# Kernel optimization log

Hardware: AMD Instinct MI355X
Metric: run time of the kernel (lower is better)

## Reference

```python
import jax, jax.numpy as jnp
import numpy as np
import math

H = 128      # hidden_size
B = 4        # bsz
N = 32       # bsz * num_doc_per_q
L = 128      # doc_len


def setup_inputs() -> dict:
    key = jax.random.key(0)
    ks = jax.random.split(key, 7)
    word_ent_info = jax.random.normal(ks[0], (N, L, H), dtype=jnp.float32)
    word_ent_info_mask = jax.random.randint(ks[1], (N, L), 0, 2, dtype=jnp.int32)
    doc = jax.random.normal(ks[2], (N, L, H), dtype=jnp.float32)
    doc_mask = jax.random.randint(ks[3], (N, L), 0, 2, dtype=jnp.int32)
    q_for_text = jax.random.normal(ks[4], (B, H), dtype=jnp.float32)
    # nn.Linear(3H, H): weight [H, 3H], bias [H]
    W1 = jax.random.normal(ks[5], (H, 3 * H), dtype=jnp.float32) / math.sqrt(3 * H)
    b1 = jnp.zeros((H,), dtype=jnp.float32)
    # nn.Linear(H, 1): weight [1, H], bias [1]
    w2 = jax.random.normal(ks[6], (1, H), dtype=jnp.float32) / math.sqrt(H)
    b2 = jnp.zeros((1,), dtype=jnp.float32)
    return {"word_ent_info": word_ent_info, "word_ent_info_mask": word_ent_info_mask,
            "doc": doc, "doc_mask": doc_mask, "q_for_text": q_for_text,
            "W1": W1, "b1": b1, "w2": w2, "b2": b2}


def reference(word_ent_info, word_ent_info_mask, doc, doc_mask, q_for_text, W1, b1, w2, b2):
    n, l, h = doc.shape
    bsz = q_for_text.shape[0]
    dt = doc.dtype

    # word_ent_infoagg = mask^T @ word_ent_info -> [N, H]
    m = word_ent_info_mask.astype(dt)
    ent_agg = jnp.einsum('nl,nlh->nh', m, word_ent_info)

    # q expanded to one row per document: [N, H]
    q_exp = jnp.repeat(q_for_text, n // bsz, axis=0)

    # Split W1 over the concat([doc_self, ent_agg, q_agg]) feature axis.
    # score_pre[n,j,k,:] = W1a @ (doc_j*doc_k) + W1b @ (doc_j*ent_agg) + W1c @ (doc_k*q)
    W1a, W1b, W1c = jnp.split(W1, 3, axis=1)        # each [H, H]
    A = jnp.einsum('nje,nke,ge->njkg', doc, doc, W1a)          # [N,L,L,H]
    Bt = jnp.einsum('nje,ge->njg', doc * ent_agg[:, None, :], W1b)  # [N,L,H]
    Ct = jnp.einsum('nke,ge->nkg', doc * q_exp[:, None, :], W1c)    # [N,L,H]
    hid = jnp.tanh(A + Bt[:, :, None, :] + Ct[:, None, :, :] + b1)  # [N,L,L,H]

    score = (jnp.einsum('njkg,g->njk', hid, w2[0]) + b2[0]) / math.sqrt(h)

    dm = doc_mask.astype(dt)
    score_mask = dm[:, :, None] * dm[:, None, :]     # [N,L,L]
    score = jnp.where(score_mask == 0.0, jnp.asarray(-1e9, dt), score)
    w = jax.nn.softmax(score, axis=-1) * score_mask
    doc_ent_enc = jnp.einsum('njk,nkh->njh', w, doc)  # [N,L,H]
    return doc_ent_enc
```

## Files before the change

### kernel.cpp

```cpp
#include <hip/hip_runtime.h>
#include <hip/hip_bf16.h>
#include <math.h>

#define Hh 128
#define Nn 32
#define Ll 128
#define W1S 384
#define PAD 136

typedef __attribute__((ext_vector_type(8))) short short8;
typedef __attribute__((ext_vector_type(4))) float floatx4;

__device__ __forceinline__ unsigned short f2bf(float x) {
  __hip_bfloat16 h = __float2bfloat16(x);
  return __builtin_bit_cast(unsigned short, h);
}
__device__ __forceinline__ float bf2f(short s) {
  unsigned int u = ((unsigned int)(unsigned short)s) << 16;
  return __builtin_bit_cast(float, u);
}
__device__ __forceinline__ short8 pack8(float4 a, float4 b) {
  short8 r;
  r[0] = (short)f2bf(a.x); r[1] = (short)f2bf(a.y);
  r[2] = (short)f2bf(a.z); r[3] = (short)f2bf(a.w);
  r[4] = (short)f2bf(b.x); r[5] = (short)f2bf(b.y);
  r[6] = (short)f2bf(b.z); r[7] = (short)f2bf(b.w);
  return r;
}

__launch_bounds__(256, 2)
__global__ void k_prep(const float* __restrict__ wei, const int* __restrict__ wmask,
                       const float* __restrict__ doc, const float* __restrict__ q,
                       const float* __restrict__ W1, const float* __restrict__ b1,
                       float* __restrict__ Bt, float* __restrict__ Ct) {
  __shared__ __align__(16) short Wsb[Hh * PAD];
  __shared__ __align__(16) short docb[64 * PAD];
  __shared__ __align__(16) float red[2][Hh];
  __shared__ __align__(16) float scale[Hh];

  int b = blockIdx.x;
  int n = b >> 2, which = (b >> 1) & 1, mh = b & 1;
  int tid = threadIdx.x;
  const float* docn = doc + (size_t)n * Ll * Hh;
  int e8 = (tid & 15) * 8;

  float4 dreg[4][2];
#pragma unroll
  for (int p = 0; p < 4; ++p) {
    int row = mh * 64 + p * 16 + (tid >> 4);
    const float4* dp = (const float4*)(docn + (size_t)row * Hh + e8);
    dreg[p][0] = dp[0]; dreg[p][1] = dp[1];
  }
#pragma unroll
  for (int p = 0; p < 8; ++p) {
    int row = p * 16 + (tid >> 4);
    const float4* wp = (const float4*)(W1 + (size_t)row * W1S + (which + 1) * Hh + e8);
    *(short8*)(Wsb + row * PAD + e8) = pack8(wp[0], wp[1]);
  }
  if (which == 1) {
    if (tid < Hh) scale[tid] = q[(n >> 3) * Hh + tid];
  } else {
    int e = tid & 127, halfl = tid >> 7;
    const float* wp = wei + (size_t)n * Ll * Hh + (size_t)halfl * 64 * Hh + e;
    const int* mp = wmask + n * Ll + halfl * 64;
    float a = 0.f;
#pragma unroll 16
    for (int l = 0; l < 64; ++l) a = fmaf((float)mp[l], wp[(size_t)l * Hh], a);
    red[halfl][e] = a;
  }
  __syncthreads();
  if (which == 0 && tid < Hh) scale[tid] = red[0][tid] + red[1][tid];
  __syncthreads();

  {
    float s[8];
#pragma unroll
    for (int i = 0; i < 8; ++i) s[i] = scale[e8 + i];
#pragma unroll
    for (int p = 0; p < 4; ++p) {
      int r = p * 16 + (tid >> 4);
      float4 a = dreg[p][0], bq = dreg[p][1];
      a.x *= s[0]; a.y *= s[1]; a.z *= s[2]; a.w *= s[3];
      bq.x *= s[4]; bq.y *= s[5]; bq.z *= s[6]; bq.w *= s[7];
      *(short8*)(docb + r * PAD + e8) = pack8(a, bq);
    }
  }
  __syncthreads();

  int lane = tid & 63, w = tid >> 6;
  int l15 = lane & 15, quad = lane >> 4;
  floatx4 acc[8];
#pragma unroll
  for (int nt = 0; nt < 8; ++nt) acc[nt] = (floatx4){0.f, 0.f, 0.f, 0.f};
#pragma unroll
  for (int c = 0; c < 4; ++c) {
    int eo = c * 32 + quad * 8;
    short8 af = *(const short8*)(docb + (w * 16 + l15) * PAD + eo);
    short8 bfr[8];
#pragma unroll
    for (int nt = 0; nt < 8; ++nt)
      bfr[nt] = *(const short8*)(Wsb + (nt * 16 + l15) * PAD + eo);
#pragma unroll
    for (int nt = 0; nt < 8; ++nt)
      acc[nt] = __builtin_amdgcn_mfma_f32_16x16x32_bf16(af, bfr[nt], acc[nt], 0, 0, 0);
  }

  float* outp = (which ? Ct : Bt) + (size_t)n * Ll * Hh;
#pragma unroll
  for (int nt = 0; nt < 8; ++nt) {
    int g = nt * 16 + l15;
    float badd = which ? 0.f : b1[g];
#pragma unroll
    for (int r = 0; r < 4; ++r) {
      int k = mh * 64 + w * 16 + quad * 4 + r;
      outp[(size_t)k * Hh + g] = acc[nt][r] + badd;
    }
  }
}

__launch_bounds__(512, 6)
__global__ void k_main(const float* __restrict__ doc, const int* __restrict__ dmask,
                       const float* __restrict__ W1,
                       const float* __restrict__ w2, const float* __restrict__ b2,
                       const float* __restrict__ Bt, const float* __restrict__ Ct,
                       float* __restrict__ out) {
  __shared__ __align__(16) short As[Hh * PAD];
  __shared__ __align__(16) float sc[Ll];
  __shared__ __align__(16) float scw[Ll];

  int bid = blockIdx.x;
  int n = bid & 31, j = bid >> 5;
  int tid = threadIdx.x;
  const float* docn = doc + (size_t)n * Ll * Hh;
  size_t orow = ((size_t)n * Ll + j) * Hh;

  if (dmask[n * Ll + j] == 0) {
    if (tid < Hh) out[orow + tid] = 0.f;
    return;
  }

  int e8 = (tid & 15) * 8;
#pragma unroll
  for (int p = 0; p < 4; ++p) {
    int row = p * 32 + (tid >> 4);
    const float4* wp = (const float4*)(W1 + (size_t)row * W1S + e8);
    *(short8*)(As + row * PAD + e8) = pack8(wp[0], wp[1]);
  }

  int lane = tid & 63, w = tid >> 6;
  int l15 = lane & 15, quad = lane >> 4;

  short8 af[4];
  {
    const float* drow = docn + (size_t)(w * 16 + l15) * Hh;
    const float* jrow = docn + (size_t)j * Hh;
#pragma unroll
    for (int c = 0; c < 4; ++c) {
      int eo = c * 32 + quad * 8;
      const float4* dp = (const float4*)(drow + eo);
      const float4* jp = (const float4*)(jrow + eo);
      float4 d0 = dp[0], d1 = dp[1];
      float4 j0 = jp[0], j1 = jp[1];
      d0.x *= j0.x; d0.y *= j0.y; d0.z *= j0.z; d0.w *= j0.w;
      d1.x *= j1.x; d1.y *= j1.y; d1.z *= j1.z; d1.w *= j1.w;
      af[c] = pack8(d0, d1);
    }
  }
  __syncthreads();

  floatx4 acc[8];
#pragma unroll
  for (int nt = 0; nt < 8; ++nt) acc[nt] = (floatx4){0.f, 0.f, 0.f, 0.f};
#pragma unroll
  for (int c = 0; c < 4; ++c) {
    int eo = c * 32 + quad * 8;
#pragma unroll
    for (int nt = 0; nt < 8; ++nt) {
      short8 bfr = *(const short8*)(As + (nt * 16 + l15) * PAD + eo);
      acc[nt] = __builtin_amdgcn_mfma_f32_16x16x32_bf16(af[c], bfr, acc[nt], 0, 0, 0);
    }
  }

  const float c2 = 2.885390081777927f;
  float bbc[8], w2r[8];
  const float* btrow = Bt + orow;
#pragma unroll
  for (int nt = 0; nt < 8; ++nt) {
    int g = nt * 16 + l15;
    bbc[nt] = btrow[g] * c2;
    w2r[nt] = w2[g];
  }
  const float* ctn = Ct + (size_t)n * Ll * Hh;
#pragma unroll
  for (int r = 0; r < 4; ++r) {
    int k = w * 16 + quad * 4 + r;
    const float* ctp = ctn + (size_t)k * Hh + l15;
    float p = 0.f;
#pragma unroll
    for (int nt = 0; nt < 8; ++nt) {
      float s = acc[nt][r] + ctp[nt * 16];
      float a2 = fmaf(s, c2, bbc[nt]);
      float e = exp2f(a2);
      float th = fmaf(-2.f, __builtin_amdgcn_rcpf(e + 1.f), 1.f);
      p = fmaf(th, w2r[nt], p);
    }
    p += __shfl_xor(p, 1);
    p += __shfl_xor(p, 2);
    p += __shfl_xor(p, 4);
    p += __shfl_xor(p, 8);
    if (l15 == 0) sc[k] = p;
  }
  __syncthreads();

  {
    float b2v = b2[0];
    const float inv = 0.088388347648318447f;
    const int* dmn = dmask + n * Ll;
    int m0 = dmn[lane], m1 = dmn[lane + 64];
    float s0 = (sc[lane] + b2v) * inv;
    float s1 = (sc[lane + 64] + b2v) * inv;
    s0 = m0 ? s0 : -1e9f;
    s1 = m1 ? s1 : -1e9f;
    float mx = fmaxf(s0, s1);
#pragma unroll
    for (int off = 32; off; off >>= 1) mx = fmaxf(mx, __shfl_xor(mx, off));
    float ex0 = __expf(s0 - mx), ex1 = __expf(s1 - mx);
    float sm = ex0 + ex1;
#pragma unroll
    for (int off = 32; off; off >>= 1) sm += __shfl_xor(sm, off);
    float rden = 1.f / sm;
    scw[lane] = m0 ? ex0 * rden : 0.f;
    scw[lane + 64] = m1 ? ex1 * rden : 0.f;
  }
  __syncthreads();

  float* ored = (float*)As;
  int halfk = tid >> 7, h = tid & 127;
  const float* dbase = docn + (size_t)halfk * 32 * Hh + h;
  float o = 0.f;
#pragma unroll 8
  for (int kk = 0; kk < 32; ++kk)
    o = fmaf(scw[halfk * 32 + kk], dbase[(size_t)kk * Hh], o);
  ored[halfk * Hh + h] = o;
  __syncthreads();
  if (tid < Ll)
    out[orow + tid] = ored[tid] + ored[Hh + tid] + ored[2 * Hh + tid] + ored[3 * Hh + tid];
}

extern "C" void kernel_launch(void* const* d_in, const int* in_sizes, int n_in,
                              void* d_out, int out_size, void* d_ws, size_t ws_size,
                              hipStream_t stream) {
  const float* wei   = (const float*)d_in[0];
  const int*   wmask = (const int*)d_in[1];
  const float* doc   = (const float*)d_in[2];
  const int*   dmask = (const int*)d_in[3];
  const float* q     = (const float*)d_in[4];
  const float* W1    = (const float*)d_in[5];
  const float* b1    = (const float*)d_in[6];
  const float* w2    = (const float*)d_in[7];
  const float* b2    = (const float*)d_in[8];
  float* out = (float*)d_out;

  float* ws = (float*)d_ws;
  float* Bt = ws;
  float* Ct = Bt + (size_t)Nn * Ll * Hh;

  k_prep<<<Nn * 4, 256, 0, stream>>>(wei, wmask, doc, q, W1, b1, Bt, Ct);
  k_main<<<Nn * Ll, 512, 0, stream>>>(doc, dmask, W1, w2, b2, Bt, Ct, out);
}
```

Before: 132.2 us.

## Compact unmasked query rows and process four per block in k_main

Each block now builds a compacted list of unmasked j rows using ballot and popcount, zero-fills masked rows, and handles up to four valid j rows. The W1a slice and the bf16 doc tile are staged into shared memory once per block, and the final weighted sum over doc is batched across four rows. This is meant to cut wasted blocks on masked rows, amortise W1/doc loading across rows, and shrink the grid from 4096 to 1024 blocks. The cost is more shared memory, lower occupancy (launch bounds 4), and extra bf16 rounding of doc before the elementwise product.

```diff
diff --git a/kernel.cpp b/kernel.cpp
--- a/kernel.cpp
+++ b/kernel.cpp
@@ -71,7 +71,6 @@
   __syncthreads();
   if (which == 0 && tid < Hh) scale[tid] = red[0][tid] + red[1][tid];
   __syncthreads();
-
   {
     float s[8];
 #pragma unroll
@@ -118,26 +117,45 @@
   }
 }
 
-__launch_bounds__(512, 6)
+__launch_bounds__(512, 4)
 __global__ void k_main(const float* __restrict__ doc, const int* __restrict__ dmask,
                        const float* __restrict__ W1,
                        const float* __restrict__ w2, const float* __restrict__ b2,
                        const float* __restrict__ Bt, const float* __restrict__ Ct,
                        float* __restrict__ out) {
   __shared__ __align__(16) short As[Hh * PAD];
-  __shared__ __align__(16) float sc[Ll];
-  __shared__ __align__(16) float scw[Ll];
+  __shared__ __align__(16) short docb[Hh * PAD];
+  __shared__ __align__(16) float sc[4][Ll];
+  __shared__ __align__(16) float scw[4][Ll];
+  __shared__ int jl[Ll], ml[Ll], cnts[4];
 
   int bid = blockIdx.x;
-  int n = bid & 31, j = bid >> 5;
+  int n = bid & 31, t = bid >> 5;
   int tid = threadIdx.x;
+  int lane = tid & 63, wv = tid >> 6;
   const float* docn = doc + (size_t)n * Ll * Hh;
-  size_t orow = ((size_t)n * Ll + j) * Hh;
-
-  if (dmask[n * Ll + j] == 0) {
-    if (tid < Hh) out[orow + tid] = 0.f;
-    return;
-  }
+  const int* dmn = dmask + n * Ll;
+
+  int jme = -1, mflag = 0, pre = 0;
+  if (wv < 2) {
+    jme = (wv << 6) + lane;
+    mflag = dmn[jme] != 0;
+    unsigned long long bal = __ballot(mflag);
+    pre = __popcll(bal & ((1ull << lane) - 1ull));
+    if (lane == 0) { int tot = __popcll(bal); cnts[wv] = tot; cnts[2 + wv] = 64 - tot; }
+  }
+  __syncthreads();
+  int cnt = cnts[0] + cnts[1];
+  if (wv == 0) { if (mflag) jl[pre] = jme; else ml[lane - pre] = jme; }
+  else if (wv == 1) { if (mflag) jl[cnts[0] + pre] = jme; else ml[cnts[2] + (lane - pre)] = jme; }
+  __syncthreads();
+
+  {
+    int rr = tid >> 7, h = tid & 127;
+    int mi = 4 * t + rr;
+    if (mi < Ll - cnt) out[((size_t)n * Ll + ml[mi]) * Hh + h] = 0.f;
+  }
+  if (4 * t >= cnt) return;
 
   int e8 = (tid & 15) * 8;
 #pragma unroll
@@ -145,106 +163,140 @@
     int row = p * 32 + (tid >> 4);
     const float4* wp = (const float4*)(W1 + (size_t)row * W1S + e8);
     *(short8*)(As + row * PAD + e8) = pack8(wp[0], wp[1]);
-  }
-
-  int lane = tid & 63, w = tid >> 6;
+    const float4* dp = (const float4*)(docn + (size_t)row * Hh + e8);
+    *(short8*)(docb + row * PAD + e8) = pack8(dp[0], dp[1]);
+  }
+  __syncthreads();
+
   int l15 = lane & 15, quad = lane >> 4;
 
-  short8 af[4];
-  {
-    const float* drow = docn + (size_t)(w * 16 + l15) * Hh;
+  short8 draw[4];
+#pragma unroll
+  for (int c = 0; c < 4; ++c)
+    draw[c] = *(const short8*)(docb + (wv * 16 + l15) * PAD + c * 32 + quad * 8);
+
+  float w2r[8];
+#pragma unroll
+  for (int nt = 0; nt < 8; ++nt) w2r[nt] = w2[nt * 16 + l15];
+
+  const float c2 = 2.885390081777927f;
+  const float* ctn = Ct + (size_t)n * Ll * Hh;
+
+  for (int jj = 0; jj < 4; ++jj) {
+    int idx = 4 * t + jj;
+    if (idx >= cnt) break;
+    int j = jl[idx];
     const float* jrow = docn + (size_t)j * Hh;
+
+    floatx4 acc[8];
+#pragma unroll
+    for (int nt = 0; nt < 8; ++nt) acc[nt] = (floatx4){0.f, 0.f, 0.f, 0.f};
 #pragma unroll
     for (int c = 0; c < 4; ++c) {
       int eo = c * 32 + quad * 8;
-      const float4* dp = (const float4*)(drow + eo);
       const float4* jp = (const float4*)(jrow + eo);
-      float4 d0 = dp[0], d1 = dp[1];
       float4 j0 = jp[0], j1 = jp[1];
-      d0.x *= j0.x; d0.y *= j0.y; d0.z *= j0.z; d0.w *= j0.w;
-      d1.x *= j1.x; d1.y *= j1.y; d1.z *= j1.z; d1.w *= j1.w;
-      af[c] = pack8(d0, d1);
-    }
-  }
-  __syncthreads();
-
-  floatx4 acc[8];
-#pragma unroll
-  for (int nt = 0; nt < 8; ++nt) acc[nt] = (floatx4){0.f, 0.f, 0.f, 0.f};
-#pragma unroll
-  for (int c = 0; c < 4; ++c) {
-    int eo = c * 32 + quad * 8;
-#pragma unroll
-    for (int nt = 0; nt < 8; ++nt) {
-      short8 bfr = *(const short8*)(As + (nt * 16 + l15) * PAD + eo);
-      acc[nt] = __builtin_amdgcn_mfma_f32_16x16x32_bf16(af[c], bfr, acc[nt], 0, 0, 0);
-    }
-  }
-
-  const float c2 = 2.885390081777927f;
-  float bbc[8], w2r[8];
-  const float* btrow = Bt + orow;
-#pragma unroll
-  for (int nt = 0; nt < 8; ++nt) {
-    int g = nt * 16 + l15;
-    bbc[nt] = btrow[g] * c2;
-    w2r[nt] = w2[g];
-  }
-  const float* ctn = Ct + (size_t)n * Ll * Hh;
-#pragma unroll
-  for (int r = 0; r < 4; ++r) {
-    int k = w * 16 + quad * 4 + r;
-    const float* ctp = ctn + (size_t)k * Hh + l15;
-    float p = 0.f;
-#pragma unroll
-    for (int nt = 0; nt < 8; ++nt) {
-      float s = acc[nt][r] + ctp[nt * 16];
-      float a2 = fmaf(s, c2, bbc[nt]);
-      float e = exp2f(a2);
-      float th = fmaf(-2.f, __builtin_amdgcn_rcpf(e + 1.f), 1.f);
-      p = fmaf(th, w2r[nt], p);
-    }
-    p += __shfl_xor(p, 1);
-    p += __shfl_xor(p, 2);
-    p += __shfl_xor(p, 4);
-    p += __shfl_xor(p, 8);
-    if (l15 == 0) sc[k] = p;
-  }
-  __syncthreads();
-
+      float4 ta, tb;
+      ta.x = bf2f(draw[c][0]) * j0.x; ta.y = bf2f(draw[c][1]) * j0.y;
+      ta.z = bf2f(draw[c][2]) * j0.z; ta.w = bf2f(draw[c][3]) * j0.w;
+      tb.x = bf2f(draw[c][4]) * j1.x; tb.y = bf2f(draw[c][5]) * j1.y;
+      tb.z = bf2f(draw[c][6]) * j1.z; tb.w = bf2f(draw[c][7]) * j1.w;
+      short8 af = pack8(ta, tb);
+#pragma unroll
+      for (int nt = 0; nt < 8; ++nt) {
+        short8 bfr = *(const short8*)(As + (nt * 16 + l15) * PAD + eo);
+        acc[nt] = __builtin_amdgcn_mfma_f32_16x16x32_bf16(af, bfr, acc[nt], 0, 0, 0);
+      }
+    }
+
+    float bbc[8];
+    const float* btrow = Bt + ((size_t)n * Ll + j) * Hh;
+#pragma unroll
+    for (int nt = 0; nt < 8; ++nt) bbc[nt] = btrow[nt * 16 + l15] * c2;
+#pragma unroll
+    for (int r = 0; r < 4; ++r) {
+      int k = wv * 16 + quad * 4 + r;
+      const float* ctp = ctn + (size_t)k * Hh + l15;
+      float p = 0.f;
+#pragma unroll
+      for (int nt = 0; nt < 8; ++nt) {
+        float s = acc[nt][r] + ctp[nt * 16];
+        float a2 = fmaf(s, c2, bbc[nt]);
+        float e = exp2f(a2);
+        float th = fmaf(-2.f, __builtin_amdgcn_rcpf(e + 1.f), 1.f);
+        p = fmaf(th, w2r[nt], p);
+      }
+      p += __shfl_xor(p, 1);
+      p += __shfl_xor(p, 2);
+      p += __shfl_xor(p, 4);
+      p += __shfl_xor(p, 8);
+      if (l15 == 0) sc[jj][k] = p;
+    }
+  }
+  __syncthreads();
+
+  if (wv < 4) {
+    int idx = 4 * t + wv;
+    if (idx < cnt) {
+      float b2v = b2[0];
+      const float inv = 0.088388347648318447f;
+      int m0 = dmn[lane], m1 = dmn[lane + 64];
+      float s0 = (sc[wv][lane] + b2v) * inv;
+      float s1 = (sc[wv][lane + 64] + b2v) * inv;
+      s0 = m0 ? s0 : -1e9f;
+      s1 = m1 ? s1 : -1e9f;
+      float mx = fmaxf(s0, s1);
+#pragma unroll
+      for (int off = 32; off; off >>= 1) mx = fmaxf(mx, __shfl_xor(mx, off));
+      float ex0 = __expf(s0 - mx), ex1 = __expf(s1 - mx);
+      float sm = ex0 + ex1;
+#pragma unroll
+      for (int off = 32; off; off >>= 1) sm += __shfl_xor(sm, off);
+      float rden = 1.f / sm;
+      scw[wv][lane] = m0 ? ex0 * rden : 0.f;
+      scw[wv][lane + 64] = m1 ? ex1 * rden : 0.f;
+    } else {
+      scw[wv][lane] = 0.f;
+      scw[wv][lane + 64] = 0.f;
+    }
+  }
+  __syncthreads();
+
+  float* ored = (float*)As;
   {
-    float b2v = b2[0];
-    const float inv = 0.088388347648318447f;
-    const int* dmn = dmask + n * Ll;
-    int m0 = dmn[lane], m1 = dmn[lane + 64];
-    float s0 = (sc[lane] + b2v) * inv;
-    float s1 = (sc[lane + 64] + b2v) * inv;
-    s0 = m0 ? s0 : -1e9f;
-    s1 = m1 ? s1 : -1e9f;
-    float mx = fmaxf(s0, s1);
-#pragma unroll
-    for (int off = 32; off; off >>= 1) mx = fmaxf(mx, __shfl_xor(mx, off));
-    float ex0 = __expf(s0 - mx), ex1 = __expf(s1 - mx);
-    float sm = ex0 + ex1;
-#pragma unroll
-    for (int off = 32; off; off >>= 1) sm += __shfl_xor(sm, off);
-    float rden = 1.f / sm;
-    scw[lane] = m0 ? ex0 * rden : 0.f;
-    scw[lane + 64] = m1 ? ex1 * rden : 0.f;
-  }
-  __syncthreads();
-
-  float* ored = (float*)As;
-  int halfk = tid >> 7, h = tid & 127;
-  const float* dbase = docn + (size_t)halfk * 32 * Hh + h;
-  float o = 0.f;
-#pragma unroll 8
-  for (int kk = 0; kk < 32; ++kk)
-    o = fmaf(scw[halfk * 32 + kk], dbase[(size_t)kk * Hh], o);
-  ored[halfk * Hh + h] = o;
-  __syncthreads();
-  if (tid < Ll)
-    out[orow + tid] = ored[tid] + ored[Hh + tid] + ored[2 * Hh + tid] + ored[3 * Hh + tid];
+    int halfk = tid >> 7, h = tid & 127;
+    const float* dbase = docn + (size_t)halfk * 32 * Hh + h;
+    float o0 = 0.f, o1 = 0.f, o2 = 0.f, o3 = 0.f;
+#pragma unroll
+    for (int k4 = 0; k4 < 8; ++k4) {
+      float4 s0 = *(const float4*)&scw[0][halfk * 32 + k4 * 4];
+      float4 s1 = *(const float4*)&scw[1][halfk * 32 + k4 * 4];
+      float4 s2 = *(const float4*)&scw[2][halfk * 32 + k4 * 4];
+      float4 s3 = *(const float4*)&scw[3][halfk * 32 + k4 * 4];
+      float d0 = dbase[(size_t)(k4 * 4 + 0) * Hh];
+      float d1 = dbase[(size_t)(k4 * 4 + 1) * Hh];
+      float d2 = dbase[(size_t)(k4 * 4 + 2) * Hh];
+      float d3 = dbase[(size_t)(k4 * 4 + 3) * Hh];
+      o0 = fmaf(s0.x, d0, o0); o0 = fmaf(s0.y, d1, o0); o0 = fmaf(s0.z, d2, o0); o0 = fmaf(s0.w, d3, o0);
+      o1 = fmaf(s1.x, d0, o1); o1 = fmaf(s1.y, d1, o1); o1 = fmaf(s1.z, d2, o1); o1 = fmaf(s1.w, d3, o1);
+      o2 = fmaf(s2.x, d0, o2); o2 = fmaf(s2.y, d1, o2); o2 = fmaf(s2.z, d2, o2); o2 = fmaf(s2.w, d3, o2);
+      o3 = fmaf(s3.x, d0, o3); o3 = fmaf(s3.y, d1, o3); o3 = fmaf(s3.z, d2, o3); o3 = fmaf(s3.w, d3, o3);
+    }
+    ored[(halfk * 4 + 0) * Hh + h] = o0;
+    ored[(halfk * 4 + 1) * Hh + h] = o1;
+    ored[(halfk * 4 + 2) * Hh + h] = o2;
+    ored[(halfk * 4 + 3) * Hh + h] = o3;
+  }
+  __syncthreads();
+  {
+    int jj2 = tid >> 7, h = tid & 127;
+    int idx = 4 * t + jj2;
+    if (idx < cnt) {
+      float v = ored[(0 * 4 + jj2) * Hh + h] + ored[(1 * 4 + jj2) * Hh + h] +
+                ored[(2 * 4 + jj2) * Hh + h] + ored[(3 * 4 + jj2) * Hh + h];
+      out[((size_t)n * Ll + jl[idx]) * Hh + h] = v;
+    }
+  }
 }
 
 extern "C" void kernel_launch(void* const* d_in, const int* in_sizes, int n_in,
@@ -266,5 +318,5 @@
   float* Ct = Bt + (size_t)Nn * Ll * Hh;
 
   k_prep<<<Nn * 4, 256, 0, stream>>>(wei, wmask, doc, q, W1, b1, Bt, Ct);
-  k_main<<<Nn * Ll, 512, 0, stream>>>(doc, dmask, W1, w2, b2, Bt, Ct, out);
-}
+  k_main<<<Nn * 32, 512, 0, stream>>>(doc, dmask, W1, w2, b2, Bt, Ct, out);
+}
```

Result: no change. 130.5 us (-1.3%).

## Stage doc and W1a in LDS as fp16 halves, compute products with packed fp16

Applied to the files above, without the earlier changes.

k_main now loads W1a and the document block into shared memory as fp16 in two 64-column chunks. Each wave forms the doc_j*doc_k products with packed fp16 vector multiplies read from LDS and feeds them to fp16 MFMA, replacing bf16 MFMA on products computed in fp32 registers. This makes the global loads coalesced row-chunk reads instead of per-lane strided rows, and uses fp16 for more mantissa precision. In exchange it adds an extra barrier and LDS traffic, and the products are formed in fp16, which risks overflow or precision loss.

```diff
diff --git a/kernel.cpp b/kernel.cpp
--- a/kernel.cpp
+++ b/kernel.cpp
@@ -7,17 +7,16 @@
 #define Ll 128
 #define W1S 384
 #define PAD 136
+#define EP 64
+#define SP 72
 
 typedef __attribute__((ext_vector_type(8))) short short8;
 typedef __attribute__((ext_vector_type(4))) float floatx4;
+typedef __attribute__((ext_vector_type(8))) _Float16 f16x8;
 
 __device__ __forceinline__ unsigned short f2bf(float x) {
   __hip_bfloat16 h = __float2bfloat16(x);
   return __builtin_bit_cast(unsigned short, h);
-}
-__device__ __forceinline__ float bf2f(short s) {
-  unsigned int u = ((unsigned int)(unsigned short)s) << 16;
-  return __builtin_bit_cast(float, u);
 }
 __device__ __forceinline__ short8 pack8(float4 a, float4 b) {
   short8 r;
@@ -25,6 +24,14 @@
   r[2] = (short)f2bf(a.z); r[3] = (short)f2bf(a.w);
   r[4] = (short)f2bf(b.x); r[5] = (short)f2bf(b.y);
   r[6] = (short)f2bf(b.z); r[7] = (short)f2bf(b.w);
+  return r;
+}
+__device__ __forceinline__ f16x8 cvt8h(float4 a, float4 b) {
+  f16x8 r;
+  r[0] = (_Float16)a.x; r[1] = (_Float16)a.y;
+  r[2] = (_Float16)a.z; r[3] = (_Float16)a.w;
+  r[4] = (_Float16)b.x; r[5] = (_Float16)b.y;
+  r[6] = (_Float16)b.z; r[7] = (_Float16)b.w;
   return r;
 }
 
@@ -71,7 +78,6 @@
   __syncthreads();
   if (which == 0 && tid < Hh) scale[tid] = red[0][tid] + red[1][tid];
   __syncthreads();
-
   {
     float s[8];
 #pragma unroll
@@ -124,7 +130,8 @@
                        const float* __restrict__ w2, const float* __restrict__ b2,
                        const float* __restrict__ Bt, const float* __restrict__ Ct,
                        float* __restrict__ out) {
-  __shared__ __align__(16) short As[Hh * PAD];
+  __shared__ __align__(16) _Float16 As[Hh * SP];
+  __shared__ __align__(16) _Float16 Bs[Hh * SP];
   __shared__ __align__(16) float sc[Ll];
   __shared__ __align__(16) float scw[Ll];
 
@@ -139,45 +146,39 @@
     return;
   }
 
-  int e8 = (tid & 15) * 8;
-#pragma unroll
-  for (int p = 0; p < 4; ++p) {
-    int row = p * 32 + (tid >> 4);
-    const float4* wp = (const float4*)(W1 + (size_t)row * W1S + e8);
-    *(short8*)(As + row * PAD + e8) = pack8(wp[0], wp[1]);
-  }
-
-  int lane = tid & 63, w = tid >> 6;
+  int lane = tid & 63, wv = tid >> 6;
   int l15 = lane & 15, quad = lane >> 4;
-
-  short8 af[4];
-  {
-    const float* drow = docn + (size_t)(w * 16 + l15) * Hh;
-    const float* jrow = docn + (size_t)j * Hh;
-#pragma unroll
-    for (int c = 0; c < 4; ++c) {
+  int grow = tid >> 2, seg = (tid & 3) * 16;
+
+  floatx4 acc[8];
+#pragma unroll
+  for (int nt = 0; nt < 8; ++nt) acc[nt] = (floatx4){0.f, 0.f, 0.f, 0.f};
+
+#pragma unroll
+  for (int p = 0; p < 2; ++p) {
+    if (p) __syncthreads();
+    {
+      const float4* dsrc = (const float4*)(docn + (size_t)grow * Hh + p * EP + seg);
+      const float4* wsrc = (const float4*)(W1 + (size_t)grow * W1S + p * EP + seg);
+      float4 d0 = dsrc[0], d1 = dsrc[1], d2 = dsrc[2], d3 = dsrc[3];
+      float4 w0 = wsrc[0], w1 = wsrc[1], w2v = wsrc[2], w3 = wsrc[3];
+      *(f16x8*)(Bs + grow * SP + seg) = cvt8h(d0, d1);
+      *(f16x8*)(Bs + grow * SP + seg + 8) = cvt8h(d2, d3);
+      *(f16x8*)(As + grow * SP + seg) = cvt8h(w0, w1);
+      *(f16x8*)(As + grow * SP + seg + 8) = cvt8h(w2v, w3);
+    }
+    __syncthreads();
+#pragma unroll
+    for (int c = 0; c < 2; ++c) {
       int eo = c * 32 + quad * 8;
-      const float4* dp = (const float4*)(drow + eo);
-      const float4* jp = (const float4*)(jrow + eo);
-      float4 d0 = dp[0], d1 = dp[1];
-      float4 j0 = jp[0], j1 = jp[1];
-      d0.x *= j0.x; d0.y *= j0.y; d0.z *= j0.z; d0.w *= j0.w;
-      d1.x *= j1.x; d1.y *= j1.y; d1.z *= j1.z; d1.w *= j1.w;
-      af[c] = pack8(d0, d1);
-    }
-  }
-  __syncthreads();
-
-  floatx4 acc[8];
-#pragma unroll
-  for (int nt = 0; nt < 8; ++nt) acc[nt] = (floatx4){0.f, 0.f, 0.f, 0.f};
-#pragma unroll
-  for (int c = 0; c < 4; ++c) {
-    int eo = c * 32 + quad * 8;
-#pragma unroll
-    for (int nt = 0; nt < 8; ++nt) {
-      short8 bfr = *(const short8*)(As + (nt * 16 + l15) * PAD + eo);
-      acc[nt] = __builtin_amdgcn_mfma_f32_16x16x32_bf16(af[c], bfr, acc[nt], 0, 0, 0);
+      f16x8 dr = *(const f16x8*)(Bs + (wv * 16 + l15) * SP + eo);
+      f16x8 jr = *(const f16x8*)(Bs + j * SP + eo);
+      f16x8 af = dr * jr;
+#pragma unroll
+      for (int nt = 0; nt < 8; ++nt) {
+        f16x8 bfr = *(const f16x8*)(As + (nt * 16 + l15) * SP + eo);
+        acc[nt] = __builtin_amdgcn_mfma_f32_16x16x32_f16(af, bfr, acc[nt], 0, 0, 0);
+      }
     }
   }
 
@@ -193,7 +194,7 @@
   const float* ctn = Ct + (size_t)n * Ll * Hh;
 #pragma unroll
   for (int r = 0; r < 4; ++r) {
-    int k = w * 16 + quad * 4 + r;
+    int k = wv * 16 + quad * 4 + r;
     const float* ctp = ctn + (size_t)k * Hh + l15;
     float p = 0.f;
 #pragma unroll
@@ -235,13 +236,13 @@
   __syncthreads();
 
   float* ored = (float*)As;
-  int halfk = tid >> 7, h = tid & 127;
-  const float* dbase = docn + (size_t)halfk * 32 * Hh + h;
+  int qk = tid >> 7, h = tid & 127;
+  const float* dbase = docn + (size_t)qk * 32 * Hh + h;
   float o = 0.f;
 #pragma unroll 8
   for (int kk = 0; kk < 32; ++kk)
-    o = fmaf(scw[halfk * 32 + kk], dbase[(size_t)kk * Hh], o);
-  ored[halfk * Hh + h] = o;
+    o = fmaf(scw[qk * 32 + kk], dbase[(size_t)kk * Hh], o);
+  ored[qk * Hh + h] = o;
   __syncthreads();
   if (tid < Ll)
     out[orow + tid] = ored[tid] + ored[Hh + tid] + ored[2 * Hh + tid] + ored[3 * Hh + tid];
```

New measurement: 124.6 us. 5.8% less time.
